# Kernel optimization log

Measured on AMD Instinct MI355X. Metric: run time of the kernel, lower is better.

Reference implementation:

```python
import jax, jax.numpy as jnp
import numpy as np

HIDDEN = 2048
HEADS = 16
HEAD_DIM = HIDDEN // HEADS
TOP_K = 256
B, N = 1, 2048


def setup_inputs() -> dict:
    key = jax.random.key(0)
    ks = jax.random.split(key, 9)
    s = 0.02
    return {
        "hidden_states": jax.random.normal(ks[0], (B, N, HIDDEN), jnp.float32),
        "Wq": jax.random.normal(ks[1], (HIDDEN, HIDDEN), jnp.float32) * s,
        "bq": jnp.zeros((HIDDEN,), jnp.float32),
        "Wk": jax.random.normal(ks[2], (HIDDEN, HIDDEN), jnp.float32) * s,
        "bk": jnp.zeros((HIDDEN,), jnp.float32),
        "Wv": jax.random.normal(ks[3], (HIDDEN, HIDDEN), jnp.float32) * s,
        "bv": jnp.zeros((HIDDEN,), jnp.float32),
        "Wo": jax.random.normal(ks[4], (HIDDEN, HIDDEN), jnp.float32) * s,
        "bo": jnp.zeros((HIDDEN,), jnp.float32),
    }


def _split_heads(x):
    b, n, _ = x.shape
    return x.reshape(b, n, HEADS, HEAD_DIM).transpose(0, 2, 1, 3)  # b h n d


def reference(hidden_states, Wq, bq, Wk, bk, Wv, bv, Wo, bo):
    scale = 1.0 / jnp.sqrt(jnp.float32(HEAD_DIM))
    q = _split_heads(hidden_states @ Wq + bq)  # [b,h,n,d]
    k = _split_heads(hidden_states @ Wk + bk)
    v = _split_heads(hidden_states @ Wv + bv)

    # Sparse path (kv_seq_length > attention_window): dense QK^T used only to rank keys.
    scores = jnp.einsum("bhnd,bhmd->bhnm", q, k) * scale  # [b,h,n,n]
    importance = scores.mean(axis=2)  # [b,h,n] aggregate over queries
    _, idx = jax.lax.top_k(importance, TOP_K)  # [b,h,k]

    # gather selected K/V (torch.gather along seq dim)
    k_sel = jnp.take_along_axis(k, idx[..., None], axis=2)  # [b,h,k,d]
    v_sel = jnp.take_along_axis(v, idx[..., None], axis=2)

    w = jax.nn.softmax(jnp.einsum("bhnd,bhkd->bhnk", q, k_sel) * scale, axis=-1)
    out = jnp.einsum("bhnk,bhkd->bhnd", w, v_sel)  # [b,h,n,d]
    out = out.transpose(0, 2, 1, 3).reshape(hidden_states.shape[0], -1, HIDDEN)
    return out @ Wo + bo
```

## Files before the change

kernel.cpp:

```cpp
#include <hip/hip_runtime.h>


typedef __attribute__((ext_vector_type(8))) short bf16x8;
typedef __attribute__((ext_vector_type(4))) float f32x4;

__device__ __forceinline__ unsigned short f2bf(float x) {
    unsigned u = __float_as_uint(x);
    u += 0x7fffu + ((u >> 16) & 1u);
    return (unsigned short)(u >> 16);
}

__device__ __forceinline__ void load_lds16(const unsigned short* g, unsigned short* l) {
    __builtin_amdgcn_global_load_lds(
        (const __attribute__((address_space(1))) unsigned int*)g,
        (__attribute__((address_space(3))) unsigned int*)l,
        16, 0, 0);
}

struct Bias3 { const float* p0; const float* p1; const float* p2; };
struct Ptr4  { const float* p[4]; };

template <bool SELECT>
__global__ __launch_bounds__(256) void gemm_bf16(
    const unsigned short* __restrict__ A, long lda, long strideA,
    const unsigned short* __restrict__ Bt, long ldb, long strideB,
    void* __restrict__ Cv, long ldc, long strideC,
    Bias3 bias, int K,
    const int* __restrict__ jpos,
    unsigned short* __restrict__ Ksel,
    unsigned short* __restrict__ VselT)
{
    __shared__ __align__(16) unsigned short As[128][32];
    __shared__ __align__(16) unsigned short Bs[128][32];

    const int tid  = threadIdx.x;
    const int lane = tid & 63;
    const int wave = tid >> 6;
    const int wm = wave >> 1, wn = wave & 1;

    const int bm = blockIdx.y * 128;
    const int bn = blockIdx.x * 128;
    const int b  = blockIdx.z;

    const unsigned short* Ab = A  + (long)b * strideA;
    const unsigned short* Bb = Bt + (long)b * strideB;

    f32x4 acc[4][4];
#pragma unroll
    for (int i = 0; i < 4; i++)
#pragma unroll
        for (int j = 0; j < 4; j++) acc[i][j] = f32x4{0.f, 0.f, 0.f, 0.f};

    const int lr = lane >> 2;
    const int lc = (lane & 3) * 8;

    for (int k0 = 0; k0 < K; k0 += 32) {
        __syncthreads();
#pragma unroll
        for (int r0 = wave * 16; r0 < 128; r0 += 64) {
            load_lds16(Ab + (long)(bm + r0 + lr) * lda + k0 + lc, &As[r0][0]);
            load_lds16(Bb + (long)(bn + r0 + lr) * ldb + k0 + lc, &Bs[r0][0]);
        }
        __syncthreads();

        bf16x8 af[4], bf[4];
#pragma unroll
        for (int s = 0; s < 4; s++)
            af[s] = *(const bf16x8*)&As[wm * 64 + s * 16 + (lane & 15)][(lane >> 4) * 8];
#pragma unroll
        for (int t = 0; t < 4; t++)
            bf[t] = *(const bf16x8*)&Bs[wn * 64 + t * 16 + (lane & 15)][(lane >> 4) * 8];
#pragma unroll
        for (int s = 0; s < 4; s++)
#pragma unroll
            for (int t = 0; t < 4; t++)
                acc[s][t] = __builtin_amdgcn_mfma_f32_16x16x32_bf16(af[s], bf[t], acc[s][t], 0, 0, 0);
    }

    const float* bp = (b == 0) ? bias.p0 : (b == 1) ? bias.p1 : bias.p2;
    float* Cf = (float*)Cv;
    unsigned short* Ch = (unsigned short*)Cv;

    if (SELECT && b != 0) {
        const int hh = bn >> 7;
        int jv[4][4];
#pragma unroll
        for (int s = 0; s < 4; s++)
#pragma unroll
            for (int r = 0; r < 4; r++)
                jv[s][r] = jpos[hh * 2048 + bm + wm * 64 + s * 16 + (lane >> 4) * 4 + r];
#pragma unroll
        for (int s = 0; s < 4; s++) {
#pragma unroll
            for (int t = 0; t < 4; t++) {
                const int col = bn + wn * 64 + t * 16 + (lane & 15);
                const int dd  = col & 127;
                const float bv = bp[col];
#pragma unroll
                for (int r = 0; r < 4; r++) {
                    const int j = jv[s][r];
                    if (j >= 0) {
                        const unsigned short h16 = f2bf(acc[s][t][r] + bv);
                        if (b == 1) Ksel [hh * 32768 + j * 128 + dd] = h16;
                        else        VselT[hh * 32768 + dd * 256 + j] = h16;
                    }
                }
            }
        }
    } else {
#pragma unroll
        for (int s = 0; s < 4; s++) {
#pragma unroll
            for (int t = 0; t < 4; t++) {
                const int col  = bn + wn * 64 + t * 16 + (lane & 15);
                const int row0 = bm + wm * 64 + s * 16 + (lane >> 4) * 4;
#pragma unroll
                for (int r = 0; r < 4; r++) {
                    const int row = row0 + r;
                    if (SELECT) Ch[(long)row * ldc + col] = f2bf(acc[s][t][r] + bp[col]);
                    else        Cf[(long)b * strideC + (long)row * ldc + col] = acc[s][t][r];
                }
            }
        }
    }
}

__global__ __launch_bounds__(256) void oreduce(const float* __restrict__ part,
                                               const float* __restrict__ bo,
                                               float* __restrict__ out) {
    const long i = ((long)blockIdx.x * 256 + threadIdx.x) * 4;
    float4 a = *(const float4*)(part + i);
    float4 b = *(const float4*)(part + 4194304 + i);
    const int col = (int)(i & 2047);
    float4 o;
    o.x = a.x + b.x + bo[col];
    o.y = a.y + b.y + bo[col + 1];
    o.z = a.z + b.z + bo[col + 2];
    o.w = a.w + b.w + bo[col + 3];
    *(float4*)(out + i) = o;
}

#define QS_OFF(c)  ((c) * 2048)
#define KS_OFF(c)  (4096 + (c) * 8192)
#define PS_OFF     0
#define VS_OFF(c)  (16896 + (c) * 4096)

__global__ __launch_bounds__(256, 2) void attn_kernel(
    const unsigned short* __restrict__ Qb,
    const unsigned short* __restrict__ Ksel,
    const unsigned short* __restrict__ VselT,
    unsigned short* __restrict__ Att)
{
    __shared__ __align__(16) unsigned short smem[25088];
    __shared__ float linv[64];

    const int tid  = threadIdx.x;
    const int lane = tid & 63;
    const int wave = tid >> 6;
    const int bm = blockIdx.x * 64;
    const int h  = blockIdx.y;
    const int lr = lane >> 2, lc = (lane & 3) * 8;

    const unsigned short* Kh = Ksel  + h * 32768;
    const unsigned short* Vh = VselT + h * 32768;

    f32x4 acc[16];
#pragma unroll
    for (int t = 0; t < 16; t++) acc[t] = f32x4{0.f, 0.f, 0.f, 0.f};

#pragma unroll
    for (int c2 = 0; c2 < 2; c2++) {
        __syncthreads();
#pragma unroll
        for (int c = 0; c < 2; c++) {
            const int k0 = c2 * 64 + c * 32;
            load_lds16(Qb + (long)(bm + wave * 16 + lr) * 2048 + h * 128 + k0 + lc,
                       &smem[QS_OFF(c) + wave * 512]);
#pragma unroll
            for (int q = 0; q < 4; q++)
                load_lds16(Kh + (wave * 64 + q * 16 + lr) * 128 + k0 + lc,
                           &smem[KS_OFF(c) + (wave * 64 + q * 16) * 32]);
        }
        __syncthreads();
#pragma unroll
        for (int kk = 0; kk < 2; kk++) {
            bf16x8 af = *(const bf16x8*)&smem[QS_OFF(kk) + (wave * 16 + (lane & 15)) * 32 + (lane >> 4) * 8];
#pragma unroll
            for (int t = 0; t < 16; t++) {
                bf16x8 bfv = *(const bf16x8*)&smem[KS_OFF(kk) + (t * 16 + (lane & 15)) * 32 + (lane >> 4) * 8];
                acc[t] = __builtin_amdgcn_mfma_f32_16x16x32_bf16(af, bfv, acc[t], 0, 0, 0);
            }
        }
    }
    __syncthreads();

    const float se = 0.08838834764831845f * 1.4426950408889634f;
#pragma unroll
    for (int r = 0; r < 4; r++) {
        float mx = -3.0e38f;
#pragma unroll
        for (int t = 0; t < 16; t++) mx = fmaxf(mx, acc[t][r]);
#pragma unroll
        for (int off = 1; off < 16; off <<= 1) mx = fmaxf(mx, __shfl_xor(mx, off));
        float sum = 0.f;
#pragma unroll
        for (int t = 0; t < 16; t++) {
            float p = exp2f((acc[t][r] - mx) * se);
            acc[t][r] = p;
            sum += p;
        }
#pragma unroll
        for (int off = 1; off < 16; off <<= 1) sum += __shfl_xor(sum, off);
        const int row = wave * 16 + (lane >> 4) * 4 + r;
#pragma unroll
        for (int t = 0; t < 16; t++)
            smem[PS_OFF + row * 264 + t * 16 + (lane & 15)] = f2bf(acc[t][r]);
        if ((lane & 15) == 0) linv[row] = 1.0f / sum;
    }

    const int wm2 = wave >> 1, wn2 = wave & 1;
    f32x4 acc2[2][4];
#pragma unroll
    for (int i = 0; i < 2; i++)
#pragma unroll
        for (int j = 0; j < 4; j++) acc2[i][j] = f32x4{0.f, 0.f, 0.f, 0.f};

#pragma unroll
    for (int c2 = 0; c2 < 4; c2++) {
#pragma unroll
        for (int c = 0; c < 2; c++) {
            const int j0 = c2 * 64 + c * 32;
#pragma unroll
            for (int q = 0; q < 2; q++)
                load_lds16(Vh + (wave * 32 + q * 16 + lr) * 256 + j0 + lc,
                           &smem[VS_OFF(c) + (wave * 32 + q * 16) * 32]);
        }
        __syncthreads();
#pragma unroll
        for (int c = 0; c < 2; c++) {
            const int j0 = c2 * 64 + c * 32;
            bf16x8 af2[2], bf2v[4];
#pragma unroll
            for (int s2 = 0; s2 < 2; s2++)
                af2[s2] = *(const bf16x8*)&smem[PS_OFF + (wm2 * 32 + s2 * 16 + (lane & 15)) * 264 + j0 + (lane >> 4) * 8];
#pragma unroll
            for (int t2 = 0; t2 < 4; t2++)
                bf2v[t2] = *(const bf16x8*)&smem[VS_OFF(c) + (wn2 * 64 + t2 * 16 + (lane & 15)) * 32 + (lane >> 4) * 8];
#pragma unroll
            for (int s2 = 0; s2 < 2; s2++)
#pragma unroll
                for (int t2 = 0; t2 < 4; t2++)
                    acc2[s2][t2] = __builtin_amdgcn_mfma_f32_16x16x32_bf16(af2[s2], bf2v[t2], acc2[s2][t2], 0, 0, 0);
        }
        __syncthreads();
    }

#pragma unroll
    for (int s2 = 0; s2 < 2; s2++) {
#pragma unroll
        for (int t2 = 0; t2 < 4; t2++) {
            const int d = wn2 * 64 + t2 * 16 + (lane & 15);
#pragma unroll
            for (int r = 0; r < 4; r++) {
                const int row = wm2 * 32 + s2 * 16 + (lane >> 4) * 4 + r;
                float v = acc2[s2][t2][r] * linv[row];
                Att[(long)(bm + row) * 2048 + h * 128 + d] = f2bf(v);
            }
        }
    }
}

__global__ __launch_bounds__(256) void prep_kernel(Ptr4 srcs, unsigned short* __restrict__ WT4,
                                                   const float* __restrict__ hs,
                                                   double* __restrict__ part) {
    const int b = blockIdx.x;
    const int tid = threadIdx.x;
    if (b < 4096) {
        __shared__ float tile[64][65];
        const int z = b >> 10, xy = b & 1023;
        const float* W = srcs.p[z];
        unsigned short* WT = WT4 + (long)z * 4194304;
        const int bx = (xy & 31) * 64;
        const int by = (xy >> 5) * 64;
        const int x = tid & 63, y = tid >> 6;
#pragma unroll
        for (int i = 0; i < 64; i += 4)
            tile[y + i][x] = W[(long)(by + y + i) * 2048 + bx + x];
        __syncthreads();
#pragma unroll
        for (int i = 0; i < 64; i += 4)
            WT[(long)(bx + y + i) * 2048 + by + x] = f2bf(tile[x][y + i]);
    } else {
        const int c = b - 4096;
        const int col = (c & 7) * 256 + tid;
        const int r0  = (c >> 3) * 32;
        double a = 0.0;
#pragma unroll 4
        for (int r = 0; r < 32; r++) a += (double)hs[(long)(r0 + r) * 2048 + col];
        part[(long)(c >> 3) * 2048 + col] = a;
    }
}

__global__ void fill_kernel(float* p, float v, long n) {
    long i = ((long)blockIdx.x * blockDim.x + threadIdx.x) * 4;
    if (i + 3 < n) { p[i] = v; p[i+1] = v; p[i+2] = v; p[i+3] = v; }
}

__global__ __launch_bounds__(256) void mean_qsum_part(const double* __restrict__ part,
                                                      const float* __restrict__ Wq,
                                                      double* __restrict__ partq) {
    __shared__ float hsb[32];
    const int j  = blockIdx.x * 256 + threadIdx.x;
    const int i0 = blockIdx.y * 32;
    if (threadIdx.x < 32) {
        double s = 0.0;
#pragma unroll 4
        for (int g = 0; g < 64; g++) s += part[(long)g * 2048 + i0 + threadIdx.x];
        hsb[threadIdx.x] = (float)(s * (1.0 / 2048.0));
    }
    __syncthreads();
    double a = 0.0;
#pragma unroll 4
    for (int r = 0; r < 32; r++)
        a += (double)hsb[r] * (double)Wq[(long)(i0 + r) * 2048 + j];
    partq[(long)blockIdx.y * 2048 + j] = a;
}

__global__ void qsum_fin(const double* __restrict__ partq, const float* __restrict__ bq,
                         float* __restrict__ qbar) {
    const int j = blockIdx.x * 64 + threadIdx.x;
    double s = (double)bq[j];
#pragma unroll 4
    for (int g = 0; g < 64; g++) s += partq[(long)g * 2048 + j];
    qbar[j] = (float)s;
}

__global__ __launch_bounds__(256) void u_kernel(const float* __restrict__ Wk,
                                                const float* __restrict__ qbar,
                                                float* __restrict__ U) {
    const int i = blockIdx.x, t = threadIdx.x;
#pragma unroll
    for (int r = 0; r < 2; r++) {
        const int e = r * 1024 + t * 4;
        float4 w = *(const float4*)(Wk + (long)i * 2048 + e);
        float4 q = *(const float4*)(qbar + e);
        float a = w.x * q.x + w.y * q.y + w.z * q.z + w.w * q.w;
#pragma unroll
        for (int off = 16; off; off >>= 1) a += __shfl_xor(a, off);
        if ((t & 31) == 0) U[(long)i * 16 + r * 8 + (t >> 5)] = a;
    }
}

__global__ __launch_bounds__(256) void cast_imp_kernel(const float* __restrict__ hs,
                                                       const float* __restrict__ U,
                                                       unsigned short* __restrict__ HSb,
                                                       float* __restrict__ imp) {
    __shared__ float row[2048];
    __shared__ float red[4][16];
    const int m = blockIdx.x, t = threadIdx.x;
    for (int i = t; i < 2048; i += 256) {
        float v = hs[(long)m * 2048 + i];
        row[i] = v;
        HSb[(long)m * 2048 + i] = f2bf(v);
    }
    __syncthreads();
    float p[16];
#pragma unroll
    for (int h = 0; h < 16; h++) p[h] = 0.f;
    for (int i = t * 8; i < t * 8 + 8; i++) {
        const float v = row[i];
        const float* u = U + i * 16;
#pragma unroll
        for (int h = 0; h < 16; h++) p[h] += v * u[h];
    }
#pragma unroll
    for (int off = 32; off; off >>= 1)
#pragma unroll
        for (int h = 0; h < 16; h++) p[h] += __shfl_down(p[h], off);
    if ((t & 63) == 0)
#pragma unroll
        for (int h = 0; h < 16; h++) red[t >> 6][h] = p[h];
    __syncthreads();
    if (t < 16)
        imp[(long)t * 2048 + m] = red[0][t] + red[1][t] + red[2][t] + red[3][t];
}

__global__ __launch_bounds__(64) void topk_jpos(const float* __restrict__ imp,
                                                int* __restrict__ jpos) {
    const int h = blockIdx.x;
    const int lane = threadIdx.x;
    unsigned u[32];
#pragma unroll
    for (int r = 0; r < 32; r++) {
        unsigned x = __float_as_uint(imp[(long)h * 2048 + r * 64 + lane]);
        u[r] = (x & 0x80000000u) ? ~x : (x | 0x80000000u);
    }
    unsigned cur = 0;
    for (int b = 31; b >= 0; b--) {
        const unsigned cand = cur | (1u << b);
        int tot = 0;
#pragma unroll
        for (int r = 0; r < 32; r++)
            tot += (int)__popcll(__ballot(u[r] >= cand));
        if (tot >= 256) cur = cand;
    }
    const unsigned long long below = (1ull << lane) - 1ull;
    int pos[32];
    int base = 0;
#pragma unroll
    for (int r = 0; r < 32; r++) {
        const bool q = u[r] > cur;
        const unsigned long long m = __ballot(q);
        pos[r] = q ? base + (int)__popcll(m & below) : -1;
        base += (int)__popcll(m);
    }
#pragma unroll
    for (int r = 0; r < 32; r++) {
        const bool q = (u[r] == cur);
        const unsigned long long m = __ballot(q);
        if (q) {
            const int p = base + (int)__popcll(m & below);
            pos[r] = (p < 256) ? p : -1;
        }
        base += (int)__popcll(m);
    }
#pragma unroll
    for (int r = 0; r < 32; r++)
        jpos[h * 2048 + r * 64 + lane] = pos[r];
}

extern "C" void kernel_launch(void* const* d_in, const int* in_sizes, int n_in,
                              void* d_out, int out_size, void* d_ws, size_t ws_size,
                              hipStream_t stream)
{
    const float* hs = (const float*)d_in[0];
    const float* Wq = (const float*)d_in[1];
    const float* bq = (const float*)d_in[2];
    const float* Wk = (const float*)d_in[3];
    const float* bk = (const float*)d_in[4];
    const float* Wv = (const float*)d_in[5];
    const float* bv = (const float*)d_in[6];
    const float* Wo = (const float*)d_in[7];
    const float* bo = (const float*)d_in[8];

    char* ws = (char*)d_ws;
    size_t off = 0;
    auto alloc = [&](size_t b) -> void* {
        void* p = ws + off;
        off = (off + b + 255) & ~(size_t)255;
        return p;
    };
    unsigned short* HSb   = (unsigned short*)alloc(8388608);
    unsigned short* WT4   = (unsigned short*)alloc(4 * 8388608);
    unsigned short* Qb    = (unsigned short*)alloc(8388608);
    unsigned short* Att   = (unsigned short*)alloc(8388608);
    unsigned short* Ksel  = (unsigned short*)alloc(1048576);
    unsigned short* VselT = (unsigned short*)alloc(1048576);
    float* Opart = (float*)alloc(2 * 16777216);
    double* part  = (double*)alloc(1048576);
    double* partq = (double*)alloc(1048576);
    float* qbar  = (float*)alloc(8192);
    float* U     = (float*)alloc(131072);
    float* imp   = (float*)alloc(131072);
    int*   jpos  = (int*)alloc(131072);

    if (off > ws_size) {
        fill_kernel<<<4096, 256, 0, stream>>>((float*)d_out, 12345.0f, (long)out_size);
        return;
    }

    unsigned short* WoT = WT4 + 3 * 4194304;

    prep_kernel<<<4608, 256, 0, stream>>>(Ptr4{{Wq, Wk, Wv, Wo}}, WT4, hs, part);

    mean_qsum_part<<<dim3(8, 64), 256, 0, stream>>>(part, Wq, partq);
    qsum_fin<<<32, 64, 0, stream>>>(partq, bq, qbar);
    u_kernel<<<2048, 256, 0, stream>>>(Wk, qbar, U);
    cast_imp_kernel<<<2048, 256, 0, stream>>>(hs, U, HSb, imp);

    topk_jpos<<<16, 64, 0, stream>>>(imp, jpos);

    gemm_bf16<true><<<dim3(16, 16, 3), 256, 0, stream>>>(
        HSb, 2048, 0, WT4, 2048, 4194304, Qb, 2048, 0,
        Bias3{bq, bk, bv}, 2048, jpos, Ksel, VselT);

    attn_kernel<<<dim3(32, 16), 256, 0, stream>>>(Qb, Ksel, VselT, Att);

    gemm_bf16<false><<<dim3(16, 16, 2), 256, 0, stream>>>(
        Att, 2048, 1024, WoT, 2048, 1024, Opart, 2048, 4194304,
        Bias3{nullptr, nullptr, nullptr}, 1024, nullptr, nullptr, nullptr);

    oreduce<<<4096, 256, 0, stream>>>(Opart, bo, (float*)d_out);
}
```

Before: 325.6 us.

## Compute K/V projections only for top-k selected rows via gathered GEMM

Top-k now emits a compact per-head index list instead of a per-position map. The fused QKV GEMM gathers only the 256 selected hidden-state rows per head for the K and V projections, instead of computing all 2048 rows and discarding most of them. Q is still computed densely. This removes most of the K/V projection FLOPs at the cost of gathered row loads and a mixed-shape grid.

```diff
diff --git a/kernel.cpp b/kernel.cpp
--- a/kernel.cpp
+++ b/kernel.cpp
@@ -17,16 +17,16 @@
         16, 0, 0);
 }
 
-struct Bias3 { const float* p0; const float* p1; const float* p2; };
 struct Ptr4  { const float* p[4]; };
 
-template <bool SELECT>
-__global__ __launch_bounds__(256) void gemm_bf16(
-    const unsigned short* __restrict__ A, long lda, long strideA,
-    const unsigned short* __restrict__ Bt, long ldb, long strideB,
-    void* __restrict__ Cv, long ldc, long strideC,
-    Bias3 bias, int K,
-    const int* __restrict__ jpos,
+__global__ __launch_bounds__(256) void gemm_qkv(
+    const unsigned short* __restrict__ HSb,
+    const unsigned short* __restrict__ WT4,
+    const float* __restrict__ bq,
+    const float* __restrict__ bk,
+    const float* __restrict__ bv,
+    const int* __restrict__ idx,
+    unsigned short* __restrict__ Qb,
     unsigned short* __restrict__ Ksel,
     unsigned short* __restrict__ VselT)
 {
@@ -37,13 +37,118 @@
     const int lane = tid & 63;
     const int wave = tid >> 6;
     const int wm = wave >> 1, wn = wave & 1;
+    const int lr = lane >> 2;
+    const int lc = (lane & 3) * 8;
+
+    const int bid = blockIdx.x;
+
+    int kv, h = 0, bm, bn;
+    const unsigned short* Bt;
+    long ar0, ar1;
+    if (bid < 64) {
+        kv = 1 + (bid >> 5);
+        const int t = bid & 31;
+        h  = t >> 1;
+        bm = (t & 1) * 128;
+        bn = h * 128;
+        Bt = WT4 + (long)kv * 4194304;
+        ar0 = idx[h * 256 + bm + wave * 16 + lr];
+        ar1 = idx[h * 256 + bm + wave * 16 + 64 + lr];
+    } else {
+        kv = 0;
+        const int t = bid - 64;
+        bm = (t >> 4) * 128;
+        bn = (t & 15) * 128;
+        Bt = WT4;
+        ar0 = bm + wave * 16 + lr;
+        ar1 = bm + wave * 16 + 64 + lr;
+    }
+
+    f32x4 acc[4][4];
+#pragma unroll
+    for (int i = 0; i < 4; i++)
+#pragma unroll
+        for (int j = 0; j < 4; j++) acc[i][j] = f32x4{0.f, 0.f, 0.f, 0.f};
+
+    for (int k0 = 0; k0 < 2048; k0 += 32) {
+        __syncthreads();
+        const int r0 = wave * 16;
+        load_lds16(HSb + ar0 * 2048 + k0 + lc, &As[r0][0]);
+        load_lds16(Bt + (long)(bn + r0 + lr) * 2048 + k0 + lc, &Bs[r0][0]);
+        load_lds16(HSb + ar1 * 2048 + k0 + lc, &As[r0 + 64][0]);
+        load_lds16(Bt + (long)(bn + r0 + 64 + lr) * 2048 + k0 + lc, &Bs[r0 + 64][0]);
+        __syncthreads();
+
+        bf16x8 af[4], bf[4];
+#pragma unroll
+        for (int s = 0; s < 4; s++)
+            af[s] = *(const bf16x8*)&As[wm * 64 + s * 16 + (lane & 15)][(lane >> 4) * 8];
+#pragma unroll
+        for (int t = 0; t < 4; t++)
+            bf[t] = *(const bf16x8*)&Bs[wn * 64 + t * 16 + (lane & 15)][(lane >> 4) * 8];
+#pragma unroll
+        for (int s = 0; s < 4; s++)
+#pragma unroll
+            for (int t = 0; t < 4; t++)
+                acc[s][t] = __builtin_amdgcn_mfma_f32_16x16x32_bf16(af[s], bf[t], acc[s][t], 0, 0, 0);
+    }
+
+    if (kv == 0) {
+#pragma unroll
+        for (int s = 0; s < 4; s++) {
+#pragma unroll
+            for (int t = 0; t < 4; t++) {
+                const int col  = bn + wn * 64 + t * 16 + (lane & 15);
+                const int row0 = bm + wm * 64 + s * 16 + (lane >> 4) * 4;
+                const float bb = bq[col];
+#pragma unroll
+                for (int r = 0; r < 4; r++)
+                    Qb[(long)(row0 + r) * 2048 + col] = f2bf(acc[s][t][r] + bb);
+            }
+        }
+    } else {
+        const float* bp = (kv == 1) ? bk : bv;
+#pragma unroll
+        for (int s = 0; s < 4; s++) {
+#pragma unroll
+            for (int t = 0; t < 4; t++) {
+                const int col = bn + wn * 64 + t * 16 + (lane & 15);
+                const int dd  = col & 127;
+                const float bb = bp[col];
+                const int j0 = bm + wm * 64 + s * 16 + (lane >> 4) * 4;
+#pragma unroll
+                for (int r = 0; r < 4; r++) {
+                    const int j = j0 + r;
+                    const unsigned short h16 = f2bf(acc[s][t][r] + bb);
+                    if (kv == 1) Ksel [h * 32768 + j * 128 + dd] = h16;
+                    else         VselT[h * 32768 + dd * 256 + j] = h16;
+                }
+            }
+        }
+    }
+}
+
+__global__ __launch_bounds__(256) void gemm_o(
+    const unsigned short* __restrict__ Att,
+    const unsigned short* __restrict__ WoT,
+    float* __restrict__ Opart)
+{
+    __shared__ __align__(16) unsigned short As[128][32];
+    __shared__ __align__(16) unsigned short Bs[128][32];
+
+    const int tid  = threadIdx.x;
+    const int lane = tid & 63;
+    const int wave = tid >> 6;
+    const int wm = wave >> 1, wn = wave & 1;
+    const int lr = lane >> 2;
+    const int lc = (lane & 3) * 8;
 
     const int bm = blockIdx.y * 128;
     const int bn = blockIdx.x * 128;
     const int b  = blockIdx.z;
 
-    const unsigned short* Ab = A  + (long)b * strideA;
-    const unsigned short* Bb = Bt + (long)b * strideB;
+    const unsigned short* Ab = Att + b * 1024;
+    const unsigned short* Bb = WoT + b * 1024;
 
     f32x4 acc[4][4];
 #pragma unroll
@@ -51,15 +156,12 @@
 #pragma unroll
         for (int j = 0; j < 4; j++) acc[i][j] = f32x4{0.f, 0.f, 0.f, 0.f};
 
-    const int lr = lane >> 2;
-    const int lc = (lane & 3) * 8;
-
-    for (int k0 = 0; k0 < K; k0 += 32) {
+    for (int k0 = 0; k0 < 1024; k0 += 32) {
         __syncthreads();
 #pragma unroll
         for (int r0 = wave * 16; r0 < 128; r0 += 64) {
-            load_lds16(Ab + (long)(bm + r0 + lr) * lda + k0 + lc, &As[r0][0]);
-            load_lds16(Bb + (long)(bn + r0 + lr) * ldb + k0 + lc, &Bs[r0][0]);
+            load_lds16(Ab + (long)(bm + r0 + lr) * 2048 + k0 + lc, &As[r0][0]);
+            load_lds16(Bb + (long)(bn + r0 + lr) * 2048 + k0 + lc, &Bs[r0][0]);
         }
         __syncthreads();
 
@@ -77,50 +179,15 @@
                 acc[s][t] = __builtin_amdgcn_mfma_f32_16x16x32_bf16(af[s], bf[t], acc[s][t], 0, 0, 0);
     }
 
-    const float* bp = (b == 0) ? bias.p0 : (b == 1) ? bias.p1 : bias.p2;
-    float* Cf = (float*)Cv;
-    unsigned short* Ch = (unsigned short*)Cv;
-
-    if (SELECT && b != 0) {
-        const int hh = bn >> 7;
-        int jv[4][4];
-#pragma unroll
-        for (int s = 0; s < 4; s++)
+#pragma unroll
+    for (int s = 0; s < 4; s++) {
+#pragma unroll
+        for (int t = 0; t < 4; t++) {
+            const int col  = bn + wn * 64 + t * 16 + (lane & 15);
+            const int row0 = bm + wm * 64 + s * 16 + (lane >> 4) * 4;
 #pragma unroll
             for (int r = 0; r < 4; r++)
-                jv[s][r] = jpos[hh * 2048 + bm + wm * 64 + s * 16 + (lane >> 4) * 4 + r];
-#pragma unroll
-        for (int s = 0; s < 4; s++) {
-#pragma unroll
-            for (int t = 0; t < 4; t++) {
-                const int col = bn + wn * 64 + t * 16 + (lane & 15);
-                const int dd  = col & 127;
-                const float bv = bp[col];
-#pragma unroll
-                for (int r = 0; r < 4; r++) {
-                    const int j = jv[s][r];
-                    if (j >= 0) {
-                        const unsigned short h16 = f2bf(acc[s][t][r] + bv);
-                        if (b == 1) Ksel [hh * 32768 + j * 128 + dd] = h16;
-                        else        VselT[hh * 32768 + dd * 256 + j] = h16;
-                    }
-                }
-            }
-        }
-    } else {
-#pragma unroll
-        for (int s = 0; s < 4; s++) {
-#pragma unroll
-            for (int t = 0; t < 4; t++) {
-                const int col  = bn + wn * 64 + t * 16 + (lane & 15);
-                const int row0 = bm + wm * 64 + s * 16 + (lane >> 4) * 4;
-#pragma unroll
-                for (int r = 0; r < 4; r++) {
-                    const int row = row0 + r;
-                    if (SELECT) Ch[(long)row * ldc + col] = f2bf(acc[s][t][r] + bp[col]);
-                    else        Cf[(long)b * strideC + (long)row * ldc + col] = acc[s][t][r];
-                }
-            }
+                Opart[(long)b * 4194304 + (long)(row0 + r) * 2048 + col] = acc[s][t][r];
         }
     }
 }
@@ -385,8 +452,8 @@
         imp[(long)t * 2048 + m] = red[0][t] + red[1][t] + red[2][t] + red[3][t];
 }
 
-__global__ __launch_bounds__(64) void topk_jpos(const float* __restrict__ imp,
-                                                int* __restrict__ jpos) {
+__global__ __launch_bounds__(64) void topk_idx(const float* __restrict__ imp,
+                                               int* __restrict__ idx) {
     const int h = blockIdx.x;
     const int lane = threadIdx.x;
     unsigned u[32];
@@ -426,7 +493,7 @@
     }
 #pragma unroll
     for (int r = 0; r < 32; r++)
-        jpos[h * 2048 + r * 64 + lane] = pos[r];
+        if (pos[r] >= 0) idx[h * 256 + pos[r]] = r * 64 + lane;
 }
 
 extern "C" void kernel_launch(void* const* d_in, const int* in_sizes, int n_in,
@@ -462,7 +529,7 @@
     float* qbar  = (float*)alloc(8192);
     float* U     = (float*)alloc(131072);
     float* imp   = (float*)alloc(131072);
-    int*   jpos  = (int*)alloc(131072);
+    int*   idx   = (int*)alloc(16384);
 
     if (off > ws_size) {
         fill_kernel<<<4096, 256, 0, stream>>>((float*)d_out, 12345.0f, (long)out_size);
@@ -478,17 +545,13 @@
     u_kernel<<<2048, 256, 0, stream>>>(Wk, qbar, U);
     cast_imp_kernel<<<2048, 256, 0, stream>>>(hs, U, HSb, imp);
 
-    topk_jpos<<<16, 64, 0, stream>>>(imp, jpos);
-
-    gemm_bf16<true><<<dim3(16, 16, 3), 256, 0, stream>>>(
-        HSb, 2048, 0, WT4, 2048, 4194304, Qb, 2048, 0,
-        Bias3{bq, bk, bv}, 2048, jpos, Ksel, VselT);
+    topk_idx<<<16, 64, 0, stream>>>(imp, idx);
+
+    gemm_qkv<<<320, 256, 0, stream>>>(HSb, WT4, bq, bk, bv, idx, Qb, Ksel, VselT);
 
     attn_kernel<<<dim3(32, 16), 256, 0, stream>>>(Qb, Ksel, VselT, Att);
 
-    gemm_bf16<false><<<dim3(16, 16, 2), 256, 0, stream>>>(
-        Att, 2048, 1024, WoT, 2048, 1024, Opart, 2048, 4194304,
-        Bias3{nullptr, nullptr, nullptr}, 1024, nullptr, nullptr, nullptr);
+    gemm_o<<<dim3(16, 16, 2), 256, 0, stream>>>(Att, WoT, Opart);
 
     oreduce<<<4096, 256, 0, stream>>>(Opart, bo, (float*)d_out);
 }
```

Result: no change. 321.0 us (-1.4%).
